# Kernel tuning notes

Hardware: AMD Instinct MI355X
Metric: run time of the kernel (lower is better)

Reference implementation:

```python
import jax, jax.numpy as jnp
import numpy as np

B, H, W, C = 16, 64, 64, 256
K, S = 4, 2  # kernel=4, stride=2 (module asserts k=4, p1=1)

def setup_inputs() -> dict:
    key = jax.random.key(0)
    kx, kw, kb = jax.random.split(key, 3)
    x = jax.random.normal(kx, (B, H, W, C), dtype=jnp.float32)
    w = jax.random.normal(kw, (K, K, 1, C), dtype=jnp.float32)  # HWIO depthwise kernel
    b = jax.random.normal(kb, (C,), dtype=jnp.float32)
    return {"x": x, "w": w, "b": b}

def reference(x, w, b):
    # Depthwise ConvTranspose2d, k=4, stride=2, padding='VALID', then crop [1:-1,1:-1]
    # (equivalent to torch ConvTranspose2d(p1=1)). Transposed conv == regular conv
    # on stride-dilated input with full padding and a spatially flipped kernel.
    c = x.shape[-1]
    k = w.shape[0]
    y = jax.lax.conv_general_dilated(
        x,
        w[::-1, ::-1],                      # flip HxW taps
        window_strides=(1, 1),
        padding=((k - 1, k - 1), (k - 1, k - 1)),
        lhs_dilation=(S, S),                # implements the transpose stride
        dimension_numbers=("NHWC", "HWIO", "NHWC"),
        feature_group_count=c,              # true depthwise (one fused pass)
    )
    y = y + b  # broadcast per-channel bias
    return y[:, 1:-1, 1:-1, :]  # crop matches [:, 1:-1, 1:-1] (p1=1)
```

## Files before the change

kernel.cpp:

```cpp
#include <hip/hip_runtime.h>


#define Hh 64
#define Ww 64
#define C4 64
#define OWs 128
#define TSTRIP 13
#define NTASK_PER_N 325
#define NBLK 1300

typedef float f4 __attribute__((ext_vector_type(4)));

__device__ __forceinline__ void fma4(f4& a, const f4& x, const f4& w) {
    a.x = fmaf(x.x, w.x, a.x);
    a.y = fmaf(x.y, w.y, a.y);
    a.z = fmaf(x.z, w.z, a.z);
    a.w = fmaf(x.w, w.w, a.w);
}

__global__ __launch_bounds__(256, 4) void dwct_kernel(
    const float* __restrict__ xp_, const float* __restrict__ wp,
    const float* __restrict__ bp, float* __restrict__ op)
{
    const int lane  = threadIdx.x & 63;
    const int wslot = threadIdx.x >> 6;

    const int q = NBLK / 8, r = NBLK % 8;
    const int xcd = blockIdx.x % 8, ord = blockIdx.x / 8;
    const int newb = (xcd < r ? xcd * (q + 1) : r * (q + 1) + (xcd - r) * q) + ord;
    const int task = newb * 4 + wslot;

    const int n   = task / NTASK_PER_N;
    const int rem = task - n * NTASK_PER_N;
    const int i   = rem / 5;
    const int s   = rem - i * 5;
    const int j0  = s * TSTRIP;

    const f4* x4 = reinterpret_cast<const f4*>(xp_);
    const f4* w4 = reinterpret_cast<const f4*>(wp);
    const f4* b4 = reinterpret_cast<const f4*>(bp);
    f4*       o4 = reinterpret_cast<f4*>(op);

    f4 wv[16];
#pragma unroll
    for (int t = 0; t < 16; ++t) wv[t] = w4[t * C4 + lane];
    const f4 bv = b4[lane];
    const f4 z  = (f4){0.f, 0.f, 0.f, 0.f};

    const bool p0 = (i > 0), p1 = (i < Hh);
    const int xb0 = n * (Hh * Ww * C4) + (i - 1) * (Ww * C4) + lane;
    const int xb1 = xb0 + Ww * C4;
    const int ob  = n * (2 * Hh * OWs * C4);
    const int orow0 = ob + (2 * i - 1) * (OWs * C4) + lane;
    const int orow1 = orow0 + OWs * C4;

    f4 xp0 = z, xp1 = z, xc0 = z, xc1 = z;
    if (j0 > 0) {
        if (p0) xp0 = x4[xb0 + (j0 - 1) * C4];
        if (p1) xp1 = x4[xb1 + (j0 - 1) * C4];
    }
    if (p0) xc0 = x4[xb0 + j0 * C4];
    if (p1) xc1 = x4[xb1 + j0 * C4];

    for (int t = 0; t < TSTRIP; ++t) {
        const int j = j0 + t;

        f4 xn0 = z, xn1 = z;
        if (j + 1 < Ww) {
            if (p0) xn0 = x4[xb0 + (j + 1) * C4];
            if (p1) xn1 = x4[xb1 + (j + 1) * C4];
        }

        f4 o00 = bv, o01 = bv, o10 = bv, o11 = bv;
        fma4(o00, xp0, wv[10]); fma4(o00, xc0, wv[8]);
        fma4(o00, xp1, wv[2]);  fma4(o00, xc1, wv[0]);

        fma4(o01, xp0, wv[11]); fma4(o01, xc0, wv[9]);
        fma4(o01, xp1, wv[3]);  fma4(o01, xc1, wv[1]);

        fma4(o10, xp0, wv[14]); fma4(o10, xc0, wv[12]);
        fma4(o10, xp1, wv[6]);  fma4(o10, xc1, wv[4]);

        fma4(o11, xp0, wv[15]); fma4(o11, xc0, wv[13]);
        fma4(o11, xp1, wv[7]);  fma4(o11, xc1, wv[5]);

        const int c0 = (2 * j - 1) * C4;
        if (p0) {
            if (j > 0)  __builtin_nontemporal_store(o00, &o4[orow0 + c0]);
            if (j < Ww) __builtin_nontemporal_store(o01, &o4[orow0 + c0 + C4]);
        }
        if (p1) {
            if (j > 0)  __builtin_nontemporal_store(o10, &o4[orow1 + c0]);
            if (j < Ww) __builtin_nontemporal_store(o11, &o4[orow1 + c0 + C4]);
        }

        xp0 = xc0; xp1 = xc1; xc0 = xn0; xc1 = xn1;
    }
}

extern "C" void kernel_launch(void* const* d_in, const int* in_sizes, int n_in,
                              void* d_out, int out_size, void* d_ws, size_t ws_size,
                              hipStream_t stream) {
    const float* x = (const float*)d_in[0];
    const float* w = (const float*)d_in[1];
    const float* b = (const float*)d_in[2];
    float* out = (float*)d_out;

    hipLaunchKernelGGL(dwct_kernel, dim3(NBLK), dim3(256), 0, stream, x, w, b, out);
}
```

Measured before the change: 60.63 us.

## Balance work by splitting flattened column-step range evenly across waves

Replaces fixed 13-step strips (1300 blocks) with a flat index range of all 67600 column steps, divided evenly among 4096 waves in 1024 blocks. Each wave walks its contiguous range and may cross row boundaries, reloading the halo at each new row. This is meant to fix load imbalance and tail effects from 1300 blocks on 256 CUs, and to simplify the XCD remap to a power-of-two block count. In exchange it adds a loop with division-based index decoding and variable-length inner runs, which may hurt unrolling.

```diff
diff --git a/kernel.cpp b/kernel.cpp
--- a/kernel.cpp
+++ b/kernel.cpp
@@ -5,9 +5,9 @@
 #define Ww 64
 #define C4 64
 #define OWs 128
-#define TSTRIP 13
-#define NTASK_PER_N 325
-#define NBLK 1300
+#define NBLK 1024
+#define TOTAL 67600
+#define LOGW 12
 
 typedef float f4 __attribute__((ext_vector_type(4)));
 
@@ -25,16 +25,12 @@
     const int lane  = threadIdx.x & 63;
     const int wslot = threadIdx.x >> 6;
 
-    const int q = NBLK / 8, r = NBLK % 8;
-    const int xcd = blockIdx.x % 8, ord = blockIdx.x / 8;
-    const int newb = (xcd < r ? xcd * (q + 1) : r * (q + 1) + (xcd - r) * q) + ord;
-    const int task = newb * 4 + wslot;
+    const int xcd = blockIdx.x & 7, ord = blockIdx.x >> 3;
+    const int newb = xcd * (NBLK / 8) + ord;
+    const unsigned wr = (unsigned)(newb * 4 + wslot);
 
-    const int n   = task / NTASK_PER_N;
-    const int rem = task - n * NTASK_PER_N;
-    const int i   = rem / 5;
-    const int s   = rem - i * 5;
-    const int j0  = s * TSTRIP;
+    int g        = (int)(((unsigned long long)wr * TOTAL) >> LOGW);
+    const int g1 = (int)(((unsigned long long)(wr + 1) * TOTAL) >> LOGW);
 
     const f4* x4 = reinterpret_cast<const f4*>(xp_);
     const f4* w4 = reinterpret_cast<const f4*>(wp);
@@ -47,54 +43,63 @@
     const f4 bv = b4[lane];
     const f4 z  = (f4){0.f, 0.f, 0.f, 0.f};
 
-    const bool p0 = (i > 0), p1 = (i < Hh);
-    const int xb0 = n * (Hh * Ww * C4) + (i - 1) * (Ww * C4) + lane;
-    const int xb1 = xb0 + Ww * C4;
-    const int ob  = n * (2 * Hh * OWs * C4);
-    const int orow0 = ob + (2 * i - 1) * (OWs * C4) + lane;
-    const int orow1 = orow0 + OWs * C4;
+    while (g < g1) {
+        int n   = g / 4225;
+        int rem = g - n * 4225;
+        int i   = rem / 65;
+        int j   = rem - i * 65;
+        int run = 65 - j;
+        if (run > g1 - g) run = g1 - g;
 
-    f4 xp0 = z, xp1 = z, xc0 = z, xc1 = z;
-    if (j0 > 0) {
-        if (p0) xp0 = x4[xb0 + (j0 - 1) * C4];
-        if (p1) xp1 = x4[xb1 + (j0 - 1) * C4];
-    }
-    if (p0) xc0 = x4[xb0 + j0 * C4];
-    if (p1) xc1 = x4[xb1 + j0 * C4];
+        const bool p0 = (i > 0), p1 = (i < Hh);
+        const int xb0 = n * (Hh * Ww * C4) + (i - 1) * (Ww * C4) + lane;
+        const int xb1 = xb0 + Ww * C4;
+        const int orow0 = n * (2 * Hh * OWs * C4) + (2 * i - 1) * (OWs * C4) + lane;
+        const int orow1 = orow0 + OWs * C4;
 
-    for (int t = 0; t < TSTRIP; ++t) {
-        const int j = j0 + t;
-
-        f4 xn0 = z, xn1 = z;
-        if (j + 1 < Ww) {
-            if (p0) xn0 = x4[xb0 + (j + 1) * C4];
-            if (p1) xn1 = x4[xb1 + (j + 1) * C4];
+        f4 xp0 = z, xp1 = z, xc0 = z, xc1 = z;
+        if (j > 0) {
+            if (p0) xp0 = x4[xb0 + (j - 1) * C4];
+            if (p1) xp1 = x4[xb1 + (j - 1) * C4];
+        }
+        if (j < Ww) {
+            if (p0) xc0 = x4[xb0 + j * C4];
+            if (p1) xc1 = x4[xb1 + j * C4];
         }
 
-        f4 o00 = bv, o01 = bv, o10 = bv, o11 = bv;
-        fma4(o00, xp0, wv[10]); fma4(o00, xc0, wv[8]);
-        fma4(o00, xp1, wv[2]);  fma4(o00, xc1, wv[0]);
+        for (int t = 0; t < run; ++t, ++j) {
+            f4 xn0 = z, xn1 = z;
+            if (j + 1 < Ww) {
+                if (p0) xn0 = x4[xb0 + (j + 1) * C4];
+                if (p1) xn1 = x4[xb1 + (j + 1) * C4];
+            }
 
-        fma4(o01, xp0, wv[11]); fma4(o01, xc0, wv[9]);
-        fma4(o01, xp1, wv[3]);  fma4(o01, xc1, wv[1]);
+            f4 o00 = bv, o01 = bv, o10 = bv, o11 = bv;
+            fma4(o00, xp0, wv[10]); fma4(o00, xc0, wv[8]);
+            fma4(o00, xp1, wv[2]);  fma4(o00, xc1, wv[0]);
 
-        fma4(o10, xp0, wv[14]); fma4(o10, xc0, wv[12]);
-        fma4(o10, xp1, wv[6]);  fma4(o10, xc1, wv[4]);
+            fma4(o01, xp0, wv[11]); fma4(o01, xc0, wv[9]);
+            fma4(o01, xp1, wv[3]);  fma4(o01, xc1, wv[1]);
 
-        fma4(o11, xp0, wv[15]); fma4(o11, xc0, wv[13]);
-        fma4(o11, xp1, wv[7]);  fma4(o11, xc1, wv[5]);
+            fma4(o10, xp0, wv[14]); fma4(o10, xc0, wv[12]);
+            fma4(o10, xp1, wv[6]);  fma4(o10, xc1, wv[4]);
 
-        const int c0 = (2 * j - 1) * C4;
-        if (p0) {
-            if (j > 0)  __builtin_nontemporal_store(o00, &o4[orow0 + c0]);
-            if (j < Ww) __builtin_nontemporal_store(o01, &o4[orow0 + c0 + C4]);
+            fma4(o11, xp0, wv[15]); fma4(o11, xc0, wv[13]);
+            fma4(o11, xp1, wv[7]);  fma4(o11, xc1, wv[5]);
+
+            const int c0 = (2 * j - 1) * C4;
+            if (p0) {
+                if (j > 0)  __builtin_nontemporal_store(o00, &o4[orow0 + c0]);
+                if (j < Ww) __builtin_nontemporal_store(o01, &o4[orow0 + c0 + C4]);
+            }
+            if (p1) {
+                if (j > 0)  __builtin_nontemporal_store(o10, &o4[orow1 + c0]);
+                if (j < Ww) __builtin_nontemporal_store(o11, &o4[orow1 + c0 + C4]);
+            }
+
+            xp0 = xc0; xp1 = xc1; xc0 = xn0; xc1 = xn1;
         }
-        if (p1) {
-            if (j > 0)  __builtin_nontemporal_store(o10, &o4[orow1 + c0]);
-            if (j < Ww) __builtin_nontemporal_store(o11, &o4[orow1 + c0 + C4]);
-        }
-
-        xp0 = xc0; xp1 = xc1; xc0 = xn0; xc1 = xn1;
+        g += run;
     }
 }
 
```

Measured after the change: 56.60 us. 1.07x faster.
